# Performance work log

Measured on AMD Instinct MI355X. Metric: run time of the kernel, lower is better.

## Reference

```python
import jax, jax.numpy as jnp
import numpy as np
import math

EMB_DIM = 3        # positional embedding dim of the implicit Hyena filter
FILTER_ORDER = 64  # hidden width of the implicit filter MLP


def rmsnorm(x, w, eps=1e-8):
    return x * jax.lax.rsqrt(jnp.mean(x * x, axis=-1, keepdims=True) + eps) * w


def _implicit_filter(L, D, mlp_w1, mlp_b1, freq1, mlp_w2, mlp_b2, freq2, mlp_w3):
    # positional embedding (emb_dim=3): [t, Re exp(-i f w), Im exp(-i f w)], bands=1
    t = jnp.linspace(0.0, 1.0, L)[:, None]                               # (L,1)
    w = 2.0 * math.pi * jnp.linspace(0.0, L - 1.0, L)[:, None] / L       # (L,1)
    f = jnp.linspace(1e-4, 0.0, 1)[None, :]                              # (1,1)
    ang = f * w
    z = jnp.concatenate([t, jnp.cos(ang), -jnp.sin(ang)], axis=-1)       # (L,3)
    # implicit filter MLP with Sin activations
    h = jnp.sin(freq1 * (z @ mlp_w1.T + mlp_b1))
    h = jnp.sin(freq2 * (h @ mlp_w2.T + mlp_b2))
    h = h @ mlp_w3.T                                                     # (L,D)
    # exponential modulation (modulate=True)
    fast, slow, target = 0.3, 1.5, 1e-2
    max_decay = math.log(target) / fast
    min_decay = math.log(target) / slow
    deltas = jnp.linspace(min_decay, max_decay, D)[None, :]              # (1,D)
    h = h * jnp.exp(-t * jnp.abs(deltas))
    return h.T                                                           # (D,L)


def _fftconv(v, k, bias):
    # causal long conv via zero-padded FFT. v: (B,D,L), k: (D,L), bias: (D,)
    L = v.shape[-1]
    n = 2 * L
    kf = jnp.fft.rfft(k, n=n) / n
    y = jnp.fft.irfft(jnp.fft.rfft(v, n=n) * kf, n=n, norm="forward")[..., :L]
    return y + v * bias[None, :, None]


def _block(x, norm_in_w, in_proj_w, in_proj_b, short_filter_w, short_filter_b,
           mlp_w1, mlp_b1, freq1, mlp_w2, mlp_b2, freq2, mlp_w3, filter_bias,
           out_proj_w, out_proj_b, norm_w, ffn_w1, ffn_b1, ffn_w2, ffn_b2):
    B, L, D = x.shape
    xn = rmsnorm(x, norm_in_w)
    # Hyena operator
    u = (xn @ in_proj_w.T + in_proj_b).transpose(0, 2, 1)                # (B,3D,L)
    uc = jax.lax.conv_general_dilated(
        u, short_filter_w, (1,), [(2, 0)],
        feature_group_count=3 * D, dimension_numbers=("NCH", "OIH", "NCH"))
    uc = uc + short_filter_b[None, :, None]                              # causal k=3 depthwise
    x0, x1, v = jnp.split(uc, 3, axis=1)                                 # (B,D,L) each
    k = _implicit_filter(L, D, mlp_w1, mlp_b1, freq1, mlp_w2, mlp_b2, freq2, mlp_w3)
    v = _fftconv(v * x1, k, filter_bias)                                 # gate, long conv
    y = (v * x0).transpose(0, 2, 1) @ out_proj_w.T + out_proj_b          # gate, out proj
    # residual + FFN
    h = y + x
    o = rmsnorm(h, norm_w)
    o = jax.nn.gelu(o @ ffn_w1.T + ffn_b1) @ ffn_w2.T + ffn_b2
    return o + h


def setup_inputs():
    key = jax.random.key(0)
    B, L, D = 4, 2048, 1024
    ks = jax.random.split(key, 12)

    def lin(k, out_d, in_d):
        return jax.random.normal(k, (out_d, in_d), jnp.float32) * (1.0 / math.sqrt(in_d))

    return {
        "x": jax.random.normal(ks[0], (B, L, D), jnp.float32),
        "norm_in_w": jnp.ones((D,), jnp.float32),
        "in_proj_w": lin(ks[1], 3 * D, D),
        "in_proj_b": jnp.zeros((3 * D,), jnp.float32),
        "short_filter_w": jax.random.normal(ks[2], (3 * D, 1, 3), jnp.float32) / math.sqrt(3.0),
        "short_filter_b": jnp.zeros((3 * D,), jnp.float32),
        "mlp_w1": lin(ks[3], FILTER_ORDER, EMB_DIM),
        "mlp_b1": jnp.zeros((FILTER_ORDER,), jnp.float32),
        "freq1": jnp.ones((FILTER_ORDER,), jnp.float32),
        "mlp_w2": lin(ks[4], FILTER_ORDER, FILTER_ORDER),
        "mlp_b2": jnp.zeros((FILTER_ORDER,), jnp.float32),
        "freq2": jnp.ones((FILTER_ORDER,), jnp.float32),
        "mlp_w3": lin(ks[5], D, FILTER_ORDER),
        "filter_bias": jax.random.normal(ks[6], (D,), jnp.float32),
        "out_proj_w": lin(ks[7], D, D),
        "out_proj_b": jnp.zeros((D,), jnp.float32),
        "norm_w": jnp.ones((D,), jnp.float32),
        "ffn_w1": lin(ks[8], 2 * D, D),
        "ffn_b1": jnp.zeros((2 * D,), jnp.float32),
        "ffn_w2": lin(ks[9], D, 2 * D),
        "ffn_b2": jnp.zeros((D,), jnp.float32),
    }


def reference(x, norm_in_w, in_proj_w, in_proj_b, short_filter_w, short_filter_b,
              mlp_w1, mlp_b1, freq1, mlp_w2, mlp_b2, freq2, mlp_w3, filter_bias,
              out_proj_w, out_proj_b, norm_w, ffn_w1, ffn_b1, ffn_w2, ffn_b2):
    return _block(x, norm_in_w, in_proj_w, in_proj_b, short_filter_w, short_filter_b,
                  mlp_w1, mlp_b1, freq1, mlp_w2, mlp_b2, freq2, mlp_w3, filter_bias,
                  out_proj_w, out_proj_b, norm_w, ffn_w1, ffn_b1, ffn_w2, ffn_b2)
```

## Files before the change

kernel.cpp:

```cpp
#include <hip/hip_runtime.h>
#include <hip/hip_bf16.h>
#include <cstddef>

#define BB 4
#define LL 2048
#define DD 1024
#define MM (BB*LL)
#define KF_STRIDE 2056

#define SWZ(a) ((a) ^ (((a) >> 4) & 12))

typedef __bf16 bf16_t;
typedef __attribute__((ext_vector_type(8))) __bf16 bf16x8;
typedef __attribute__((ext_vector_type(4))) __bf16 bf16x4;
typedef __attribute__((ext_vector_type(4))) float f32x4;

#define GLD_LDS16(gp, lp) __builtin_amdgcn_global_load_lds(                 \
    (const __attribute__((address_space(1))) unsigned int*)(gp),            \
    (__attribute__((address_space(3))) unsigned int*)(lp), 16, 0, 0)

__device__ __forceinline__ float gelu_tanh(float x) {
    const float c = 0.7978845608028654f;
    float t = tanhf(c * (x + 0.044715f * x * x * x));
    return 0.5f * x * (1.0f + t);
}

__device__ __forceinline__ float2 cmul(float2 a, float2 b) {
    return make_float2(a.x * b.x - a.y * b.y, a.x * b.y + a.y * b.x);
}
__device__ __forceinline__ float2 cadd(float2 a, float2 b) {
    return make_float2(a.x + b.x, a.y + b.y);
}
__device__ __forceinline__ float2 csub(float2 a, float2 b) {
    return make_float2(a.x - b.x, a.y - b.y);
}
__device__ __forceinline__ float2 cmuli(float2 z, float s) {
    return make_float2(-s * z.y, s * z.x);
}

__global__ __launch_bounds__(256) void cast_all_kernel(
    const float* __restrict__ s0, const float* __restrict__ s1,
    const float* __restrict__ s2, const float* __restrict__ s3,
    bf16_t* __restrict__ d0, bf16_t* __restrict__ d1,
    bf16_t* __restrict__ d2, bf16_t* __restrict__ d3)
{
    const int b = blockIdx.x;
    const float* s; bf16_t* d; int base;
    if (b < 3072)      { s = s0; d = d0; base = b; }
    else if (b < 4096) { s = s1; d = d1; base = b - 3072; }
    else if (b < 6144) { s = s2; d = d2; base = b - 4096; }
    else               { s = s3; d = d3; base = b - 6144; }
    const int i = (base * 256 + threadIdx.x) * 4;
    const float4 v = *(const float4*)(s + i);
    bf16x4 o;
    o[0] = (bf16_t)v.x; o[1] = (bf16_t)v.y; o[2] = (bf16_t)v.z; o[3] = (bf16_t)v.w;
    *(bf16x4*)(d + i) = o;
}

__global__ __launch_bounds__(256) void rmsnorm_bf16_kernel(
    const float* __restrict__ in, const float* __restrict__ w,
    bf16_t* __restrict__ out)
{
    const int row = blockIdx.x;
    const float4* ip = (const float4*)(in + (size_t)row * DD);
    float4 v = ip[threadIdx.x];
    float ss = v.x*v.x + v.y*v.y + v.z*v.z + v.w*v.w;
    #pragma unroll
    for (int off = 32; off > 0; off >>= 1) ss += __shfl_down(ss, off, 64);
    __shared__ float sums[4];
    const int wid = threadIdx.x >> 6;
    if ((threadIdx.x & 63) == 0) sums[wid] = ss;
    __syncthreads();
    const float tot = sums[0] + sums[1] + sums[2] + sums[3];
    const float scale = rsqrtf(tot * (1.0f / (float)DD) + 1e-8f);
    const float4 wv = ((const float4*)w)[threadIdx.x];
    bf16x4 o;
    o[0] = (bf16_t)(v.x * scale * wv.x);
    o[1] = (bf16_t)(v.y * scale * wv.y);
    o[2] = (bf16_t)(v.z * scale * wv.z);
    o[3] = (bf16_t)(v.w * scale * wv.w);
    *(bf16x4*)(out + (size_t)row * DD + threadIdx.x * 4) = o;
}

template<int EPI, bool BF16OUT, bool BIASROW = false>
__global__ __launch_bounds__(512) void gemm_mfma_kernel(
    const bf16_t* __restrict__ A,
    const bf16_t* __restrict__ W,
    const float* __restrict__ bias,
    const float* __restrict__ res,
    float* __restrict__ Cf,
    bf16_t* __restrict__ Cb,
    int M, int N, int K)
{
    __shared__ __align__(16) bf16_t As[2][128 * 64];
    __shared__ __align__(16) bf16_t Ws[2][128 * 64];
    const int tid  = threadIdx.x;
    const int bm   = blockIdx.y * 128;
    const int bn   = blockIdx.x * 128;
    const int lane = tid & 63;
    const int wave = tid >> 6;
    const int wr   = (wave >> 2) * 64;
    const int wc   = (wave & 3) * 32;

    int srow[2], sqg[2];
    #pragma unroll
    for (int c = 0; c < 2; ++c) {
        const int p = c * 512 + tid;
        srow[c] = p >> 3;
        sqg[c]  = (((p & 7) ^ (srow[c] & 7)) << 3);
    }

    f32x4 acc[4][2] = {};

    const int fr = lane & 15;
    const int fc = (lane >> 4) * 8;

    const int nt = K >> 6;

    #pragma unroll
    for (int c = 0; c < 2; ++c) {
        GLD_LDS16(A + (size_t)(bm + srow[c]) * K + sqg[c],
                  &As[0][c * 4096 + tid * 8]);
        GLD_LDS16(W + (size_t)(bn + srow[c]) * K + sqg[c],
                  &Ws[0][c * 4096 + tid * 8]);
    }
    __syncthreads();

    int cur = 0;
    for (int t = 0; t < nt; ++t) {
        if (t + 1 < nt) {
            const int k0 = (t + 1) << 6;
            #pragma unroll
            for (int c = 0; c < 2; ++c) {
                GLD_LDS16(A + (size_t)(bm + srow[c]) * K + k0 + sqg[c],
                          &As[cur ^ 1][c * 4096 + tid * 8]);
                GLD_LDS16(W + (size_t)(bn + srow[c]) * K + k0 + sqg[c],
                          &Ws[cur ^ 1][c * 4096 + tid * 8]);
            }
        }
        #pragma unroll
        for (int ks = 0; ks < 64; ks += 32) {
            const int q = (ks + fc) >> 3;
            bf16x8 af[4], wf[2];
            #pragma unroll
            for (int i = 0; i < 4; ++i) {
                const int r = wr + i*16 + fr;
                af[i] = *(const bf16x8*)(&As[cur][r * 64 + ((q ^ (r & 7)) << 3)]);
            }
            #pragma unroll
            for (int j = 0; j < 2; ++j) {
                const int r = wc + j*16 + fr;
                wf[j] = *(const bf16x8*)(&Ws[cur][r * 64 + ((q ^ (r & 7)) << 3)]);
            }
            __builtin_amdgcn_s_setprio(1);
            #pragma unroll
            for (int i = 0; i < 4; ++i)
                #pragma unroll
                for (int j = 0; j < 2; ++j)
                    acc[i][j] = __builtin_amdgcn_mfma_f32_16x16x32_bf16(
                        af[i], wf[j], acc[i][j], 0, 0, 0);
            __builtin_amdgcn_s_setprio(0);
        }
        __syncthreads();
        cur ^= 1;
    }

    const int fq = lane >> 4;
    #pragma unroll
    for (int i = 0; i < 4; ++i) {
        const int row0 = bm + wr + i*16 + fq*4;
        #pragma unroll
        for (int j = 0; j < 2; ++j) {
            const int col = bn + wc + j*16 + fr;
            const float bcol = BIASROW ? 0.0f : bias[col];
            #pragma unroll
            for (int r = 0; r < 4; ++r) {
                float v = acc[i][j][r] + (BIASROW ? bias[row0 + r] : bcol);
                if constexpr (EPI == 2) v = gelu_tanh(v);
                if constexpr (EPI == 1) v += res[(size_t)(row0 + r) * N + col];
                if constexpr (BF16OUT)
                    Cb[(size_t)(row0 + r) * N + col] = (bf16_t)v;
                else
                    Cf[(size_t)(row0 + r) * N + col] = v;
            }
        }
    }
}

__global__ __launch_bounds__(256) void shortfilter_kernel(
    const bf16_t* __restrict__ ut, const float* __restrict__ sw,
    const float* __restrict__ sb, bf16_t* __restrict__ x0t,
    float* __restrict__ vin)
{
    const int d = blockIdx.x;
    const int c0 = d, c1 = DD + d, c2 = 2 * DD + d;
    const float w0a = sw[c0*3+0], w0b = sw[c0*3+1], w0c = sw[c0*3+2], b0 = sb[c0];
    const float w1a = sw[c1*3+0], w1b = sw[c1*3+1], w1c = sw[c1*3+2], b1 = sb[c1];
    const float w2a = sw[c2*3+0], w2b = sw[c2*3+1], w2c = sw[c2*3+2], b2 = sb[c2];
    const bf16_t* r0 = ut + (size_t)c0 * MM;
    const bf16_t* r1 = ut + (size_t)c1 * MM;
    const bf16_t* r2 = ut + (size_t)c2 * MM;
    bf16_t* o0 = x0t + (size_t)d * MM;
    float*  o1 = vin + (size_t)d * MM;
    for (int m0 = threadIdx.x * 8; m0 < MM; m0 += 2048) {
        const int l0 = m0 & (LL - 1);
        const bf16x8 a0 = *(const bf16x8*)(r0 + m0);
        const bf16x8 a1 = *(const bf16x8*)(r1 + m0);
        const bf16x8 a2 = *(const bf16x8*)(r2 + m0);
        float u0[10], u1[10], u2[10];
        u0[0] = u0[1] = u1[0] = u1[1] = u2[0] = u2[1] = 0.0f;
        if (l0 != 0) {
            u0[0] = (float)r0[m0-2]; u0[1] = (float)r0[m0-1];
            u1[0] = (float)r1[m0-2]; u1[1] = (float)r1[m0-1];
            u2[0] = (float)r2[m0-2]; u2[1] = (float)r2[m0-1];
        }
        #pragma unroll
        for (int i = 0; i < 8; ++i) {
            u0[i+2] = (float)a0[i];
            u1[i+2] = (float)a1[i];
            u2[i+2] = (float)a2[i];
        }
        bf16x8 ov;
        float v1o[8];
        #pragma unroll
        for (int i = 0; i < 8; ++i) {
            const float v0 = w0c*u0[i+2] + w0b*u0[i+1] + w0a*u0[i] + b0;
            const float v1 = w1c*u1[i+2] + w1b*u1[i+1] + w1a*u1[i] + b1;
            const float v2 = w2c*u2[i+2] + w2b*u2[i+1] + w2a*u2[i] + b2;
            ov[i] = (bf16_t)v0;
            v1o[i] = v2 * v1;
        }
        *(bf16x8*)(o0 + m0) = ov;
        *(float4*)(o1 + m0)     = make_float4(v1o[0], v1o[1], v1o[2], v1o[3]);
        *(float4*)(o1 + m0 + 4) = make_float4(v1o[4], v1o[5], v1o[6], v1o[7]);
    }
}

__global__ __launch_bounds__(256) void filtermlp_kernel(
    const float* __restrict__ w1, const float* __restrict__ b1,
    const float* __restrict__ f1, const float* __restrict__ w2,
    const float* __restrict__ b2, const float* __restrict__ f2,
    float* __restrict__ h2t)
{
    __shared__ float w2s[64 * 64];
    __shared__ float h1s[64][32];
    const int tid = threadIdx.x;
    #pragma unroll
    for (int i = 0; i < 4; ++i)
        ((float4*)w2s)[tid + 256 * i] = ((const float4*)w2)[tid + 256 * i];

    const int l0 = blockIdx.x * 32;
    const int l  = tid & 31;
    const float fl = (float)(l0 + l);
    const float t   = fl * (1.0f / (float)(LL - 1));
    const float ang = 1e-4f * 6.283185307179586f * fl * (1.0f / (float)LL);
    const float z0 = t, z1 = cosf(ang), z2 = -sinf(ang);

    #pragma unroll
    for (int i = 0; i < 8; ++i) {
        const int j = (tid >> 5) + 8 * i;
        const float s = w1[j*3+0]*z0 + w1[j*3+1]*z1 + w1[j*3+2]*z2 + b1[j];
        h1s[j][l] = sinf(f1[j] * s);
    }
    __syncthreads();

    const int jb = (tid >> 5) * 8;
    float acc[8];
    #pragma unroll
    for (int i = 0; i < 8; ++i) acc[i] = b2[jb + i];
    #pragma unroll
    for (int jj = 0; jj < 64; jj += 4) {
        const float h0 = h1s[jj + 0][l];
        const float h1v = h1s[jj + 1][l];
        const float h2v = h1s[jj + 2][l];
        const float h3 = h1s[jj + 3][l];
        #pragma unroll
        for (int i = 0; i < 8; ++i) {
            const float4 wv = *(const float4*)&w2s[(jb + i) * 64 + jj];
            acc[i] += wv.x * h0 + wv.y * h1v + wv.z * h2v + wv.w * h3;
        }
    }
    #pragma unroll
    for (int i = 0; i < 8; ++i)
        h2t[(size_t)(jb + i) * LL + l0 + l] = sinf(f2[jb + i] * acc[i]);
}

__global__ __launch_bounds__(256) void filtermod_kernel(
    const float* __restrict__ w3, const float* __restrict__ h2t,
    float* __restrict__ kfilt)
{
    __shared__ float w3s[32 * 64];
    const int d0 = blockIdx.y * 32;
    const int l  = blockIdx.x * 256 + threadIdx.x;
    for (int i = threadIdx.x; i < 32 * 64; i += 256) w3s[i] = w3[d0 * 64 + i];
    __syncthreads();
    float acc[32] = {};
    for (int j = 0; j < 64; ++j) {
        const float v = h2t[j * LL + l];
        #pragma unroll
        for (int dd = 0; dd < 32; ++dd) acc[dd] += w3s[dd*64 + j] * v;
    }
    const float t = (float)l / (float)(LL - 1);
    const float min_decay = -3.0701134573253944f;
    const float max_decay = -15.350567286626972f;
    #pragma unroll
    for (int dd = 0; dd < 32; ++dd) {
        const int d = d0 + dd;
        const float delta = fabsf(min_decay + (max_decay - min_decay) * (float)d / (float)(DD - 1));
        kfilt[(size_t)d * LL + l] = acc[dd] * expf(-t * delta);
    }
}

template<int SIGN>
__device__ __forceinline__ void fft4096_r8_ip(float2* __restrict__ buf)
{
    const float fs = (float)SIGN;
    const float RH = 0.7071067811865476f;
    const int tid = threadIdx.x;
    #pragma unroll
    for (int t = 0; t < 4; ++t) {
        const int ls = 3 * t;
        const int s  = 1 << ls;
        const float theta = fs * 6.283185307179586f / (float)(4096 >> ls);
        float2 a[8];
        #pragma unroll
        for (int m = 0; m < 8; ++m) a[m] = buf[SWZ(tid + m * 512)];
        __syncthreads();
        const int p = tid >> ls;
        const int q = tid & (s - 1);
        float sn, cs;
        __sincosf(theta * (float)p, &sn, &cs);
        const float2 W1 = make_float2(cs, sn);
        const float2 W2 = cmul(W1, W1);
        const float2 W3 = cmul(W2, W1);
        const float2 W4 = cmul(W2, W2);
        const float2 W5 = cmul(W4, W1);
        const float2 W6 = cmul(W4, W2);
        const float2 W7 = cmul(W4, W3);
        const float2 es = cadd(a[0], a[4]), ed = csub(a[0], a[4]);
        const float2 fs2 = cadd(a[2], a[6]), fd = csub(a[2], a[6]);
        const float2 E0 = cadd(es, fs2);
        const float2 E1 = cadd(ed, cmuli(fd, fs));
        const float2 E2 = csub(es, fs2);
        const float2 E3 = csub(ed, cmuli(fd, fs));
        const float2 os = cadd(a[1], a[5]), od = csub(a[1], a[5]);
        const float2 gs = cadd(a[3], a[7]), gd = csub(a[3], a[7]);
        const float2 O0 = cadd(os, gs);
        const float2 O1 = cadd(od, cmuli(gd, fs));
        const float2 O2 = csub(os, gs);
        const float2 O3 = csub(od, cmuli(gd, fs));
        const float2 T0 = O0;
        const float2 T1 = make_float2(RH * (O1.x - fs * O1.y), RH * (fs * O1.x + O1.y));
        const float2 T2 = cmuli(O2, fs);
        const float2 T3 = make_float2(RH * (-O3.x - fs * O3.y), RH * (fs * O3.x - O3.y));
        const int o = q + (p << (ls + 3));
        buf[SWZ(o)]         = cadd(E0, T0);
        buf[SWZ(o + s)]     = cmul(W1, cadd(E1, T1));
        buf[SWZ(o + 2*s)]   = cmul(W2, cadd(E2, T2));
        buf[SWZ(o + 3*s)]   = cmul(W3, cadd(E3, T3));
        buf[SWZ(o + 4*s)]   = cmul(W4, csub(E0, T0));
        buf[SWZ(o + 5*s)]   = cmul(W5, csub(E1, T1));
        buf[SWZ(o + 6*s)]   = cmul(W6, csub(E2, T2));
        buf[SWZ(o + 7*s)]   = cmul(W7, csub(E3, T3));
        __syncthreads();
    }
}

__global__ __launch_bounds__(512, 4) void kfft_kernel(
    const float* __restrict__ kfilt, float2* __restrict__ Kf)
{
    __shared__ float2 fb[4096];
    const int d0 = blockIdx.x * 2;
    const float* k0 = kfilt + (size_t)d0 * LL;
    const float* k1 = k0 + LL;
    const float inv = 1.0f / 4096.0f;
    const int tid = threadIdx.x;
    for (int i = tid; i < 2048; i += 512) {
        fb[SWZ(i)]        = make_float2(k0[i] * inv, k1[i] * inv);
        fb[SWZ(i + 2048)] = make_float2(0.f, 0.f);
    }
    __syncthreads();
    fft4096_r8_ip<-1>(fb);
    float2* o0 = Kf + (size_t)d0 * KF_STRIDE;
    float2* o1 = o0 + KF_STRIDE;
    for (int k = tid; k <= 2048; k += 512) {
        const float2 z1 = fb[SWZ(k)];
        const float2 z2 = fb[SWZ((4096 - k) & 4095)];
        o0[k] = make_float2(0.5f * (z1.x + z2.x), 0.5f * (z1.y - z2.y));
        o1[k] = make_float2(0.5f * (z1.y + z2.y), 0.5f * (z2.x - z1.x));
    }
}

__global__ __launch_bounds__(512, 4) void fftconv_kernel(
    float* __restrict__ vio, const float2* __restrict__ Kf,
    const float* __restrict__ fbias)
{
    __shared__ float2 fb[4096];
    const int blk = blockIdx.x;
    const int d   = blk >> 1;
    float* v1 = vio + (size_t)(2 * blk) * LL;
    float* v2 = v1 + LL;
    const int tid = threadIdx.x;
    for (int i = tid; i < 2048; i += 512) {
        fb[SWZ(i)]        = make_float2(v1[i], v2[i]);
        fb[SWZ(i + 2048)] = make_float2(0.f, 0.f);
    }
    __syncthreads();
    fft4096_r8_ip<-1>(fb);
    const float2* kf = Kf + (size_t)d * KF_STRIDE;
    for (int i = tid; i < 4096; i += 512) {
        float2 k;
        if (i <= 2048) k = kf[i];
        else { const float2 t = kf[4096 - i]; k = make_float2(t.x, -t.y); }
        fb[SWZ(i)] = cmul(fb[SWZ(i)], k);
    }
    __syncthreads();
    fft4096_r8_ip<1>(fb);
    const float bias = fbias[d];
    for (int i = tid; i < 2048; i += 512) {
        const float2 zy = fb[SWZ(i)];
        v1[i] = zy.x + bias * v1[i];
        v2[i] = zy.y + bias * v2[i];
    }
}

__global__ __launch_bounds__(256) void gate_transpose_kernel(
    const float* __restrict__ y, const bf16_t* __restrict__ x0t,
    bf16_t* __restrict__ g)
{
    __shared__ float tile[32][33];
    const int b  = blockIdx.z;
    const int l0 = blockIdx.x * 32;
    const int d0 = blockIdx.y * 32;
    const int tx  = threadIdx.x & 31;
    const int tyb = threadIdx.x >> 5;
    #pragma unroll
    for (int i = 0; i < 4; ++i) {
        const int dy = tyb + i * 8;
        const size_t src = ((size_t)(d0 + dy) * BB + b) * LL + l0 + tx;
        tile[dy][tx] = y[src] * (float)x0t[src];
    }
    __syncthreads();
    #pragma unroll
    for (int i = 0; i < 4; ++i) {
        const int ly = tyb + i * 8;
        g[((size_t)(b * LL + l0 + ly)) * DD + d0 + tx] = (bf16_t)tile[tx][ly];
    }
}

extern "C" void kernel_launch(void* const* d_in, const int* in_sizes, int n_in,
                              void* d_out, int out_size, void* d_ws, size_t ws_size,
                              hipStream_t stream)
{
    (void)in_sizes; (void)n_in; (void)out_size; (void)ws_size;
    const float* x   = (const float*)d_in[0];
    const float* nw0 = (const float*)d_in[1];
    const float* ipw = (const float*)d_in[2];
    const float* ipb = (const float*)d_in[3];
    const float* sfw = (const float*)d_in[4];
    const float* sfb = (const float*)d_in[5];
    const float* w1  = (const float*)d_in[6];
    const float* b1  = (const float*)d_in[7];
    const float* f1  = (const float*)d_in[8];
    const float* w2  = (const float*)d_in[9];
    const float* b2  = (const float*)d_in[10];
    const float* f2  = (const float*)d_in[11];
    const float* w3  = (const float*)d_in[12];
    const float* fbv = (const float*)d_in[13];
    const float* opw = (const float*)d_in[14];
    const float* opb = (const float*)d_in[15];
    const float* nw1 = (const float*)d_in[16];
    const float* fw1 = (const float*)d_in[17];
    const float* fb1 = (const float*)d_in[18];
    const float* fw2 = (const float*)d_in[19];
    const float* fb2 = (const float*)d_in[20];
    float* out = (float*)d_out;

    float* ws = (float*)d_ws;
    bf16_t* utb    = (bf16_t*)ws;
    bf16_t* gatedb = (bf16_t*)ws;
    float*  h      = ws + 4194304;
    bf16_t* midb   = (bf16_t*)(ws + 12582912);
    bf16_t* xnb    = (bf16_t*)(ws + 25165824);
    bf16_t* x0tb   = (bf16_t*)(ws + 29360128);
    float*  vio    = ws + 37748736;
    float*  kfilt  = ws + 46137344;
    float2* Kf     = (float2*)(ws + 48234496);
    bf16_t* ipwb   = (bf16_t*)(ws + 52445184);
    bf16_t* opwb   = ipwb + 3145728;
    bf16_t* fw1b   = opwb + 1048576;
    bf16_t* fw2b   = fw1b + 2097152;
    float*  h2t    = ws + 56639488;

    cast_all_kernel<<<8192, 256, 0, stream>>>(ipw, opw, fw1, fw2,
                                              ipwb, opwb, fw1b, fw2b);
    filtermlp_kernel<<<LL/32, 256, 0, stream>>>(w1, b1, f1, w2, b2, f2, h2t);
    filtermod_kernel<<<dim3(LL/256, DD/32), 256, 0, stream>>>(w3, h2t, kfilt);
    kfft_kernel<<<DD/2, 512, 0, stream>>>(kfilt, Kf);
    rmsnorm_bf16_kernel<<<MM, 256, 0, stream>>>(x, nw0, xnb);
    gemm_mfma_kernel<0, true, true><<<dim3(MM/128, 3072/128), 512, 0, stream>>>(
        ipwb, xnb, ipb, nullptr, nullptr, utb, 3*DD, MM, DD);
    shortfilter_kernel<<<DD, 256, 0, stream>>>(utb, sfw, sfb, x0tb, vio);
    fftconv_kernel<<<BB*DD/2, 512, 0, stream>>>(vio, Kf, fbv);
    gate_transpose_kernel<<<dim3(LL/32, DD/32, BB), 256, 0, stream>>>(vio, x0tb, gatedb);
    gemm_mfma_kernel<1, false><<<dim3(DD/128, MM/128), 512, 0, stream>>>(
        gatedb, opwb, opb, x, h, nullptr, MM, DD, DD);
    rmsnorm_bf16_kernel<<<MM, 256, 0, stream>>>(h, nw1, xnb);
    gemm_mfma_kernel<2, true><<<dim3(2*DD/128, MM/128), 512, 0, stream>>>(
        xnb, fw1b, fb1, nullptr, nullptr, midb, MM, 2*DD, DD);
    gemm_mfma_kernel<1, false><<<dim3(DD/128, MM/128), 512, 0, stream>>>(
        midb, fw2b, fb2, h, out, nullptr, MM, DD, 2*DD);
}
```

Measured before the change: 475.2 us.

## Precompute FFT twiddle table and add 256-thread GEMM variant for FFN down-projection

Adds a small kernel that precomputes a 4096-entry twiddle table, and the FFT stages now load twiddles from global memory instead of computing them with sincos and chained complex multiplies. Separately, a 256-thread GEMM variant with a 64x64 tile per wave is introduced and used only for the final FFN down-projection (K=2048). This trades twiddle arithmetic for gathered global loads and gives each wave more MFMA work per LDS fetch, at the cost of higher register pressure and possibly lower occupancy.

```diff
diff --git a/kernel.cpp b/kernel.cpp
--- a/kernel.cpp
+++ b/kernel.cpp
@@ -57,6 +57,14 @@
     *(bf16x4*)(d + i) = o;
 }
 
+__global__ __launch_bounds__(256) void twiddle_kernel(float2* __restrict__ tw)
+{
+    const int i = blockIdx.x * 256 + threadIdx.x;
+    float sn, cs;
+    __sincosf(-6.283185307179586f * (float)i / 4096.0f, &sn, &cs);
+    tw[i] = make_float2(cs, sn);
+}
+
 __global__ __launch_bounds__(256) void rmsnorm_bf16_kernel(
     const float* __restrict__ in, const float* __restrict__ w,
     bf16_t* __restrict__ out)
@@ -83,7 +91,7 @@
 }
 
 template<int EPI, bool BF16OUT, bool BIASROW = false>
-__global__ __launch_bounds__(512) void gemm_mfma_kernel(
+__global__ __launch_bounds__(512) void gemm_mfma_k512(
     const bf16_t* __restrict__ A,
     const bf16_t* __restrict__ W,
     const float* __restrict__ bias,
@@ -171,6 +179,111 @@
         const int row0 = bm + wr + i*16 + fq*4;
         #pragma unroll
         for (int j = 0; j < 2; ++j) {
+            const int col = bn + wc + j*16 + fr;
+            const float bcol = BIASROW ? 0.0f : bias[col];
+            #pragma unroll
+            for (int r = 0; r < 4; ++r) {
+                float v = acc[i][j][r] + (BIASROW ? bias[row0 + r] : bcol);
+                if constexpr (EPI == 2) v = gelu_tanh(v);
+                if constexpr (EPI == 1) v += res[(size_t)(row0 + r) * N + col];
+                if constexpr (BF16OUT)
+                    Cb[(size_t)(row0 + r) * N + col] = (bf16_t)v;
+                else
+                    Cf[(size_t)(row0 + r) * N + col] = v;
+            }
+        }
+    }
+}
+
+template<int EPI, bool BF16OUT, bool BIASROW = false>
+__global__ __launch_bounds__(256) void gemm_mfma_k256(
+    const bf16_t* __restrict__ A,
+    const bf16_t* __restrict__ W,
+    const float* __restrict__ bias,
+    const float* __restrict__ res,
+    float* __restrict__ Cf,
+    bf16_t* __restrict__ Cb,
+    int M, int N, int K)
+{
+    __shared__ __align__(16) bf16_t As[2][128 * 64];
+    __shared__ __align__(16) bf16_t Ws[2][128 * 64];
+    const int tid  = threadIdx.x;
+    const int bm   = blockIdx.y * 128;
+    const int bn   = blockIdx.x * 128;
+    const int lane = tid & 63;
+    const int wave = tid >> 6;
+    const int wr   = (wave >> 1) * 64;
+    const int wc   = (wave & 1) * 64;
+
+    int srow[4], sqg[4];
+    #pragma unroll
+    for (int c = 0; c < 4; ++c) {
+        const int p = c * 256 + tid;
+        srow[c] = p >> 3;
+        sqg[c]  = (((p & 7) ^ (srow[c] & 7)) << 3);
+    }
+
+    f32x4 acc[4][4] = {};
+
+    const int fr = lane & 15;
+    const int fc = (lane >> 4) * 8;
+
+    const int nt = K >> 6;
+
+    #pragma unroll
+    for (int c = 0; c < 4; ++c) {
+        GLD_LDS16(A + (size_t)(bm + srow[c]) * K + sqg[c],
+                  &As[0][c * 2048 + tid * 8]);
+        GLD_LDS16(W + (size_t)(bn + srow[c]) * K + sqg[c],
+                  &Ws[0][c * 2048 + tid * 8]);
+    }
+    __syncthreads();
+
+    int cur = 0;
+    for (int t = 0; t < nt; ++t) {
+        if (t + 1 < nt) {
+            const int k0 = (t + 1) << 6;
+            #pragma unroll
+            for (int c = 0; c < 4; ++c) {
+                GLD_LDS16(A + (size_t)(bm + srow[c]) * K + k0 + sqg[c],
+                          &As[cur ^ 1][c * 2048 + tid * 8]);
+                GLD_LDS16(W + (size_t)(bn + srow[c]) * K + k0 + sqg[c],
+                          &Ws[cur ^ 1][c * 2048 + tid * 8]);
+            }
+        }
+        #pragma unroll
+        for (int ks = 0; ks < 64; ks += 32) {
+            const int q = (ks + fc) >> 3;
+            bf16x8 af[4], wf[4];
+            #pragma unroll
+            for (int i = 0; i < 4; ++i) {
+                const int r = wr + i*16 + fr;
+                af[i] = *(const bf16x8*)(&As[cur][r * 64 + ((q ^ (r & 7)) << 3)]);
+            }
+            #pragma unroll
+            for (int j = 0; j < 4; ++j) {
+                const int r = wc + j*16 + fr;
+                wf[j] = *(const bf16x8*)(&Ws[cur][r * 64 + ((q ^ (r & 7)) << 3)]);
+            }
+            __builtin_amdgcn_s_setprio(1);
+            #pragma unroll
+            for (int i = 0; i < 4; ++i)
+                #pragma unroll
+                for (int j = 0; j < 4; ++j)
+                    acc[i][j] = __builtin_amdgcn_mfma_f32_16x16x32_bf16(
+                        af[i], wf[j], acc[i][j], 0, 0, 0);
+            __builtin_amdgcn_s_setprio(0);
+        }
+        __syncthreads();
+        cur ^= 1;
+    }
+
+    const int fq = lane >> 4;
+    #pragma unroll
+    for (int i = 0; i < 4; ++i) {
+        const int row0 = bm + wr + i*16 + fq*4;
+        #pragma unroll
+        for (int j = 0; j < 4; ++j) {
             const int col = bn + wc + j*16 + fr;
             const float bcol = BIASROW ? 0.0f : bias[col];
             #pragma unroll
@@ -312,7 +425,8 @@
 }
 
 template<int SIGN>
-__device__ __forceinline__ void fft4096_r8_ip(float2* __restrict__ buf)
+__device__ __forceinline__ void fft4096_r8_ip(
+    float2* __restrict__ buf, const float2* __restrict__ tw)
 {
     const float fs = (float)SIGN;
     const float RH = 0.7071067811865476f;
@@ -321,22 +435,21 @@
     for (int t = 0; t < 4; ++t) {
         const int ls = 3 * t;
         const int s  = 1 << ls;
-        const float theta = fs * 6.283185307179586f / (float)(4096 >> ls);
         float2 a[8];
         #pragma unroll
         for (int m = 0; m < 8; ++m) a[m] = buf[SWZ(tid + m * 512)];
         __syncthreads();
         const int p = tid >> ls;
         const int q = tid & (s - 1);
-        float sn, cs;
-        __sincosf(theta * (float)p, &sn, &cs);
-        const float2 W1 = make_float2(cs, sn);
-        const float2 W2 = cmul(W1, W1);
-        const float2 W3 = cmul(W2, W1);
-        const float2 W4 = cmul(W2, W2);
-        const float2 W5 = cmul(W4, W1);
-        const float2 W6 = cmul(W4, W2);
-        const float2 W7 = cmul(W4, W3);
+        const int pls = (p << ls) & 4095;
+        float2 W[8];
+        int idx = 0;
+        #pragma unroll
+        for (int m = 1; m < 8; ++m) {
+            idx = (idx + pls) & 4095;
+            const float2 w = tw[idx];
+            W[m] = make_float2(w.x, (SIGN > 0) ? -w.y : w.y);
+        }
         const float2 es = cadd(a[0], a[4]), ed = csub(a[0], a[4]);
         const float2 fs2 = cadd(a[2], a[6]), fd = csub(a[2], a[6]);
         const float2 E0 = cadd(es, fs2);
@@ -355,19 +468,20 @@
         const float2 T3 = make_float2(RH * (-O3.x - fs * O3.y), RH * (fs * O3.x - O3.y));
         const int o = q + (p << (ls + 3));
         buf[SWZ(o)]         = cadd(E0, T0);
-        buf[SWZ(o + s)]     = cmul(W1, cadd(E1, T1));
-        buf[SWZ(o + 2*s)]   = cmul(W2, cadd(E2, T2));
-        buf[SWZ(o + 3*s)]   = cmul(W3, cadd(E3, T3));
-        buf[SWZ(o + 4*s)]   = cmul(W4, csub(E0, T0));
-        buf[SWZ(o + 5*s)]   = cmul(W5, csub(E1, T1));
-        buf[SWZ(o + 6*s)]   = cmul(W6, csub(E2, T2));
-        buf[SWZ(o + 7*s)]   = cmul(W7, csub(E3, T3));
+        buf[SWZ(o + s)]     = cmul(W[1], cadd(E1, T1));
+        buf[SWZ(o + 2*s)]   = cmul(W[2], cadd(E2, T2));
+        buf[SWZ(o + 3*s)]   = cmul(W[3], cadd(E3, T3));
+        buf[SWZ(o + 4*s)]   = cmul(W[4], csub(E0, T0));
+        buf[SWZ(o + 5*s)]   = cmul(W[5], csub(E1, T1));
+        buf[SWZ(o + 6*s)]   = cmul(W[6], csub(E2, T2));
+        buf[SWZ(o + 7*s)]   = cmul(W[7], csub(E3, T3));
         __syncthreads();
     }
 }
 
 __global__ __launch_bounds__(512, 4) void kfft_kernel(
-    const float* __restrict__ kfilt, float2* __restrict__ Kf)
+    const float* __restrict__ kfilt, float2* __restrict__ Kf,
+    const float2* __restrict__ tw)
 {
     __shared__ float2 fb[4096];
     const int d0 = blockIdx.x * 2;
@@ -380,7 +494,7 @@
         fb[SWZ(i + 2048)] = make_float2(0.f, 0.f);
     }
     __syncthreads();
-    fft4096_r8_ip<-1>(fb);
+    fft4096_r8_ip<-1>(fb, tw);
     float2* o0 = Kf + (size_t)d0 * KF_STRIDE;
     float2* o1 = o0 + KF_STRIDE;
     for (int k = tid; k <= 2048; k += 512) {
@@ -393,7 +507,7 @@
 
 __global__ __launch_bounds__(512, 4) void fftconv_kernel(
     float* __restrict__ vio, const float2* __restrict__ Kf,
-    const float* __restrict__ fbias)
+    const float* __restrict__ fbias, const float2* __restrict__ tw)
 {
     __shared__ float2 fb[4096];
     const int blk = blockIdx.x;
@@ -406,7 +520,7 @@
         fb[SWZ(i + 2048)] = make_float2(0.f, 0.f);
     }
     __syncthreads();
-    fft4096_r8_ip<-1>(fb);
+    fft4096_r8_ip<-1>(fb, tw);
     const float2* kf = Kf + (size_t)d * KF_STRIDE;
     for (int i = tid; i < 4096; i += 512) {
         float2 k;
@@ -415,7 +529,7 @@
         fb[SWZ(i)] = cmul(fb[SWZ(i)], k);
     }
     __syncthreads();
-    fft4096_r8_ip<1>(fb);
+    fft4096_r8_ip<1>(fb, tw);
     const float bias = fbias[d];
     for (int i = tid; i < 2048; i += 512) {
         const float2 zy = fb[SWZ(i)];
@@ -481,6 +595,7 @@
     bf16_t* gatedb = (bf16_t*)ws;
     float*  h      = ws + 4194304;
     bf16_t* midb   = (bf16_t*)(ws + 12582912);
+    float2* tw     = (float2*)(ws + 20971520);
     bf16_t* xnb    = (bf16_t*)(ws + 25165824);
     bf16_t* x0tb   = (bf16_t*)(ws + 29360128);
     float*  vio    = ws + 37748736;
@@ -494,20 +609,21 @@
 
     cast_all_kernel<<<8192, 256, 0, stream>>>(ipw, opw, fw1, fw2,
                                               ipwb, opwb, fw1b, fw2b);
+    twiddle_kernel<<<16, 256, 0, stream>>>(tw);
     filtermlp_kernel<<<LL/32, 256, 0, stream>>>(w1, b1, f1, w2, b2, f2, h2t);
     filtermod_kernel<<<dim3(LL/256, DD/32), 256, 0, stream>>>(w3, h2t, kfilt);
-    kfft_kernel<<<DD/2, 512, 0, stream>>>(kfilt, Kf);
+    kfft_kernel<<<DD/2, 512, 0, stream>>>(kfilt, Kf, tw);
     rmsnorm_bf16_kernel<<<MM, 256, 0, stream>>>(x, nw0, xnb);
-    gemm_mfma_kernel<0, true, true><<<dim3(MM/128, 3072/128), 512, 0, stream>>>(
+    gemm_mfma_k512<0, true, true><<<dim3(MM/128, 3072/128), 512, 0, stream>>>(
         ipwb, xnb, ipb, nullptr, nullptr, utb, 3*DD, MM, DD);
     shortfilter_kernel<<<DD, 256, 0, stream>>>(utb, sfw, sfb, x0tb, vio);
-    fftconv_kernel<<<BB*DD/2, 512, 0, stream>>>(vio, Kf, fbv);
+    fftconv_kernel<<<BB*DD/2, 512, 0, stream>>>(vio, Kf, fbv, tw);
     gate_transpose_kernel<<<dim3(LL/32, DD/32, BB), 256, 0, stream>>>(vio, x0tb, gatedb);
-    gemm_mfma_kernel<1, false><<<dim3(DD/128, MM/128), 512, 0, stream>>>(
+    gemm_mfma_k512<1, false><<<dim3(DD/128, MM/128), 512, 0, stream>>>(
         gatedb, opwb, opb, x, h, nullptr, MM, DD, DD);
     rmsnorm_bf16_kernel<<<MM, 256, 0, stream>>>(h, nw1, xnb);
-    gemm_mfma_kernel<2, true><<<dim3(2*DD/128, MM/128), 512, 0, stream>>>(
+    gemm_mfma_k512<2, true><<<dim3(2*DD/128, MM/128), 512, 0, stream>>>(
         xnb, fw1b, fb1, nullptr, nullptr, midb, MM, 2*DD, DD);
-    gemm_mfma_kernel<1, false><<<dim3(DD/128, MM/128), 512, 0, stream>>>(
+    gemm_mfma_k256<1, false><<<dim3(DD/128, MM/128), 256, 0, stream>>>(
         midb, fw2b, fb2, h, out, nullptr, MM, DD, 2*DD);
 }
```

Result: no change. 478.8 us (+0.8%).
